# Kernel tuning notes

Hardware: AMD Instinct MI355X
Metric: run time of the kernel (lower is better)

## Reference

```python
import jax, jax.numpy as jnp
import numpy as np

EPS = 1e-10


def setup_inputs() -> dict:
    key = jax.random.key(0)
    k1, k2 = jax.random.split(key)
    supports = jax.random.normal(k1, (32, 512, 1024), dtype=jnp.float32)
    targets = jax.random.normal(k2, (32, 512, 1024), dtype=jnp.float32)
    return {"supports": supports, "targets": targets}


def reference(supports, targets):
    # targets: [B, T, D], supports: [B, S, D] -> sim: [B, T, S]
    # F.cosine_similarity(a, b, eps): dot / max(||a||*||b||, eps)
    dots = jnp.einsum("btd,bsd->bts", targets, supports)
    t_norm = jnp.linalg.norm(targets, axis=-1)   # [B, T]
    s_norm = jnp.linalg.norm(supports, axis=-1)  # [B, S]
    denom = jnp.maximum(t_norm[:, :, None] * s_norm[:, None, :], EPS)
    sim = dots / denom
    # normalize=True default: map (-1, 1) -> (0, 1)
    return (sim + 1.0) * 0.5
```

## Files before the change

### kernel.cpp

```cpp
#include <hip/hip_runtime.h>
#include <hip/hip_bf16.h>

typedef __attribute__((ext_vector_type(8))) short short8;
typedef __attribute__((ext_vector_type(4))) float f32x4;

#define NBATCH 32
#define NT 512
#define NS 512
#define ND 1024
#define BM 128
#define BN 256
#define BK 32
#define NK (ND / BK)

__device__ __forceinline__ short f2bf(float f) {
    union { __hip_bfloat16 h; short s; } u;
    u.h = __float2bfloat16(f);
    return u.s;
}

__device__ __forceinline__ short8 cvt8(float4 a, float4 b) {
    short8 r;
    r[0] = f2bf(a.x); r[1] = f2bf(a.y); r[2] = f2bf(a.z); r[3] = f2bf(a.w);
    r[4] = f2bf(b.x); r[5] = f2bf(b.y); r[6] = f2bf(b.z); r[7] = f2bf(b.w);
    return r;
}

__device__ __forceinline__ float ssq4(float s, float4 a) {
    return fmaf(a.x, a.x, fmaf(a.y, a.y, fmaf(a.z, a.z, fmaf(a.w, a.w, s))));
}

__global__ __launch_bounds__(512, 2)
void paircos_mfma(const float* __restrict__ sup, const float* __restrict__ tgt,
                  float* __restrict__ out) {
    __shared__ __align__(16) short As[2][BM * BK];
    __shared__ __align__(16) short Bs[2][BN * BK];
    __shared__ float tn[BM];
    __shared__ float sn[BN];

    const int tid = threadIdx.x;
    const int l    = blockIdx.x;
    const int wgid = (l & 7) * 32 + (l >> 3);
    const int b    = wgid >> 3;
    const int til  = wgid & 7;
    const int bt0  = (til >> 1) * BM;
    const int bs0  = (til & 1) * BN;

    const int seg  = tid & 3;
    const int srow = tid >> 2;

    const float* gA = tgt + (size_t)b * NT * ND + (size_t)(bt0 + srow) * ND + seg * 8;
    const float* gB = sup + (size_t)b * NS * ND + (size_t)(bs0 + srow) * ND + seg * 8;

    const int wave = tid >> 6;
    const int lane = tid & 63;
    const int wr  = (wave >> 2) * 64;
    const int wc  = (wave & 3) * 64;
    const int lhi = lane >> 4;
    const int llo = lane & 15;

    f32x4 acc[4][4];
#pragma unroll
    for (int m = 0; m < 4; ++m)
#pragma unroll
        for (int n = 0; n < 4; ++n)
            acc[m][n] = (f32x4){0.f, 0.f, 0.f, 0.f};

    float sqa = 0.f, sqb0 = 0.f, sqb1 = 0.f;

    float4 pA0, pA1, pB0, pB1, pB2, pB3;

    const int pu   = ((seg + (srow >> 1)) & 3) * 8;
    const int offw = srow * BK + pu;

#define LOADT(KK)                                                              \
    do {                                                                       \
        pA0 = *reinterpret_cast<const float4*>(gA + (KK) * BK);                \
        pA1 = *reinterpret_cast<const float4*>(gA + (KK) * BK + 4);            \
        pB0 = *reinterpret_cast<const float4*>(gB + (KK) * BK);                \
        pB1 = *reinterpret_cast<const float4*>(gB + (KK) * BK + 4);            \
        pB2 = *reinterpret_cast<const float4*>(gB + (KK) * BK + 128 * ND);     \
        pB3 = *reinterpret_cast<const float4*>(gB + (KK) * BK + 128 * ND + 4); \
    } while (0)

#define STORET(P)                                                              \
    do {                                                                       \
        sqa  = ssq4(ssq4(sqa,  pA0), pA1);                                     \
        *reinterpret_cast<short8*>(&As[P][offw]) = cvt8(pA0, pA1);             \
        sqb0 = ssq4(ssq4(sqb0, pB0), pB1);                                     \
        *reinterpret_cast<short8*>(&Bs[P][offw]) = cvt8(pB0, pB1);             \
        sqb1 = ssq4(ssq4(sqb1, pB2), pB3);                                     \
        *reinterpret_cast<short8*>(&Bs[P][offw + 128 * BK]) = cvt8(pB2, pB3);  \
    } while (0)

#define FRAG_READ(P)                                                           \
    do {                                                                       \
        _Pragma("unroll") for (int m = 0; m < 4; ++m) {                        \
            const int row = wr + m * 16 + llo;                                 \
            const int off = row * BK + (((lhi + (row >> 1)) & 3) * 8);         \
            af[m] = *reinterpret_cast<const short8*>(&As[P][off]);             \
        }                                                                      \
        _Pragma("unroll") for (int n = 0; n < 4; ++n) {                        \
            const int row = wc + n * 16 + llo;                                 \
            const int off = row * BK + (((lhi + (row >> 1)) & 3) * 8);         \
            bfr[n] = *reinterpret_cast<const short8*>(&Bs[P][off]);            \
        }                                                                      \
    } while (0)

#define MFMA_BLOCK()                                                           \
    do {                                                                       \
        __builtin_amdgcn_s_setprio(1);                                         \
        _Pragma("unroll") for (int m = 0; m < 4; ++m)                          \
            _Pragma("unroll") for (int n = 0; n < 4; ++n)                      \
                acc[m][n] = __builtin_amdgcn_mfma_f32_16x16x32_bf16(           \
                    af[m], bfr[n], acc[m][n], 0, 0, 0);                        \
        __builtin_amdgcn_s_setprio(0);                                         \
    } while (0)

#define PHASE_FENCE()                                                          \
    do {                                                                       \
        asm volatile("s_waitcnt lgkmcnt(0)" ::: "memory");                     \
        __builtin_amdgcn_s_barrier();                                          \
        asm volatile("" ::: "memory");                                         \
    } while (0)

    LOADT(0);
    STORET(0);
    LOADT(1);
    PHASE_FENCE();

    for (int k = 0; k < NK; ++k) {
        const int cur = k & 1;
        short8 af[4], bfr[4];
        FRAG_READ(cur);
        if (k + 1 < NK) STORET(cur ^ 1);
        if (k + 2 < NK) LOADT(k + 2);
        MFMA_BLOCK();
        PHASE_FENCE();
    }

    sqa  += __shfl_xor(sqa, 1);
    sqa  += __shfl_xor(sqa, 2);
    sqb0 += __shfl_xor(sqb0, 1);
    sqb0 += __shfl_xor(sqb0, 2);
    sqb1 += __shfl_xor(sqb1, 1);
    sqb1 += __shfl_xor(sqb1, 2);
    if (seg == 0) {
        tn[srow]       = sqrtf(sqa);
        sn[srow]       = sqrtf(sqb0);
        sn[srow + 128] = sqrtf(sqb1);
    }
    __syncthreads();

    float* outp = out + (size_t)b * NT * NS;
#pragma unroll
    for (int m = 0; m < 4; ++m) {
        const int lr0 = wr + m * 16 + lhi * 4;
#pragma unroll
        for (int n = 0; n < 4; ++n) {
            const int lc = wc + n * 16 + llo;
            const float snv = sn[lc];
            const int col = bs0 + lc;
#pragma unroll
            for (int j = 0; j < 4; ++j) {
                const float denom = fmaxf(tn[lr0 + j] * snv, 1e-10f);
                outp[(size_t)(bt0 + lr0 + j) * NS + col] =
                    acc[m][n][j] / denom * 0.5f + 0.5f;
            }
        }
    }
}

extern "C" void kernel_launch(void* const* d_in, const int* in_sizes, int n_in,
                              void* d_out, int out_size, void* d_ws, size_t ws_size,
                              hipStream_t stream) {
    const float* sup = (const float*)d_in[0];
    const float* tgt = (const float*)d_in[1];
    float* out = (float*)d_out;
    (void)in_sizes; (void)n_in; (void)out_size; (void)d_ws; (void)ws_size;
    paircos_mfma<<<dim3(32 * 8), 512, 0, stream>>>(sup, tgt, out);
}
```

Measured before the change: 35.15 us.

## Triple-buffer LDS and prefetch MFMA fragments one step ahead

Moves the K-loop from double to triple LDS buffering and reads the next tile's fragments into registers before issuing the current tile's MFMAs, unrolling by two with ping-pong register sets. The goal is to hide LDS read latency behind the MFMA chain, so the matrix core no longer waits on ds_read at the start of each step. This adds 50% more shared memory and an extra set of fragment registers, which could hurt occupancy at the requested two blocks per CU.

```diff
diff --git a/kernel.cpp b/kernel.cpp
--- a/kernel.cpp
+++ b/kernel.cpp
@@ -12,6 +12,8 @@
 #define BN 256
 #define BK 32
 #define NK (ND / BK)
+#define ATSZ (BM * BK)
+#define BTSZ (BN * BK)
 
 __device__ __forceinline__ short f2bf(float f) {
     union { __hip_bfloat16 h; short s; } u;
@@ -33,8 +35,8 @@
 __global__ __launch_bounds__(512, 2)
 void paircos_mfma(const float* __restrict__ sup, const float* __restrict__ tgt,
                   float* __restrict__ out) {
-    __shared__ __align__(16) short As[2][BM * BK];
-    __shared__ __align__(16) short Bs[2][BN * BK];
+    __shared__ __align__(16) short As[3 * ATSZ];
+    __shared__ __align__(16) short Bs[3 * BTSZ];
     __shared__ float tn[BM];
     __shared__ float sn[BN];
 
@@ -69,6 +71,7 @@
     float sqa = 0.f, sqb0 = 0.f, sqb1 = 0.f;
 
     float4 pA0, pA1, pB0, pB1, pB2, pB3;
+    short8 xa[4], xb[4], ya[4], yb[4];
 
     const int pu   = ((seg + (srow >> 1)) & 3) * 8;
     const int offw = srow * BK + pu;
@@ -83,37 +86,38 @@
         pB3 = *reinterpret_cast<const float4*>(gB + (KK) * BK + 128 * ND + 4); \
     } while (0)
 
-#define STORET(P)                                                              \
+#define STORET(WB)                                                             \
     do {                                                                       \
         sqa  = ssq4(ssq4(sqa,  pA0), pA1);                                     \
-        *reinterpret_cast<short8*>(&As[P][offw]) = cvt8(pA0, pA1);             \
+        *reinterpret_cast<short8*>(&As[(WB) * ATSZ + offw]) = cvt8(pA0, pA1);  \
         sqb0 = ssq4(ssq4(sqb0, pB0), pB1);                                     \
-        *reinterpret_cast<short8*>(&Bs[P][offw]) = cvt8(pB0, pB1);             \
+        *reinterpret_cast<short8*>(&Bs[(WB) * BTSZ + offw]) = cvt8(pB0, pB1);  \
         sqb1 = ssq4(ssq4(sqb1, pB2), pB3);                                     \
-        *reinterpret_cast<short8*>(&Bs[P][offw + 128 * BK]) = cvt8(pB2, pB3);  \
+        *reinterpret_cast<short8*>(&Bs[(WB) * BTSZ + offw + 128 * BK]) =       \
+            cvt8(pB2, pB3);                                                    \
     } while (0)
 
-#define FRAG_READ(P)                                                           \
+#define FRAG_READ(FA, FB, RB)                                                  \
     do {                                                                       \
         _Pragma("unroll") for (int m = 0; m < 4; ++m) {                        \
             const int row = wr + m * 16 + llo;                                 \
-            const int off = row * BK + (((lhi + (row >> 1)) & 3) * 8);         \
-            af[m] = *reinterpret_cast<const short8*>(&As[P][off]);             \
+            const int off = (RB) * ATSZ + row * BK + (((lhi + (row >> 1)) & 3) * 8); \
+            FA[m] = *reinterpret_cast<const short8*>(&As[off]);                \
         }                                                                      \
         _Pragma("unroll") for (int n = 0; n < 4; ++n) {                        \
             const int row = wc + n * 16 + llo;                                 \
-            const int off = row * BK + (((lhi + (row >> 1)) & 3) * 8);         \
-            bfr[n] = *reinterpret_cast<const short8*>(&Bs[P][off]);            \
+            const int off = (RB) * BTSZ + row * BK + (((lhi + (row >> 1)) & 3) * 8); \
+            FB[n] = *reinterpret_cast<const short8*>(&Bs[off]);                \
         }                                                                      \
     } while (0)
 
-#define MFMA_BLOCK()                                                           \
+#define MFMA_BLOCK(FA, FB)                                                     \
     do {                                                                       \
         __builtin_amdgcn_s_setprio(1);                                         \
         _Pragma("unroll") for (int m = 0; m < 4; ++m)                          \
             _Pragma("unroll") for (int n = 0; n < 4; ++n)                      \
                 acc[m][n] = __builtin_amdgcn_mfma_f32_16x16x32_bf16(           \
-                    af[m], bfr[n], acc[m][n], 0, 0, 0);                        \
+                    FA[m], FB[n], acc[m][n], 0, 0, 0);                         \
         __builtin_amdgcn_s_setprio(0);                                         \
     } while (0)
 
@@ -124,19 +128,32 @@
         asm volatile("" ::: "memory");                                         \
     } while (0)
 
+#define ROTATE()                                                               \
+    do { int t_ = cbuf; cbuf = rbuf; rbuf = wbuf; wbuf = t_; } while (0)
+
     LOADT(0);
     STORET(0);
     LOADT(1);
     PHASE_FENCE();
+    STORET(1);
+    LOADT(2);
+    FRAG_READ(xa, xb, 0);
+    PHASE_FENCE();
+    int cbuf = 0, rbuf = 1, wbuf = 2;
 
-    for (int k = 0; k < NK; ++k) {
-        const int cur = k & 1;
-        short8 af[4], bfr[4];
-        FRAG_READ(cur);
-        if (k + 1 < NK) STORET(cur ^ 1);
-        if (k + 2 < NK) LOADT(k + 2);
-        MFMA_BLOCK();
+    for (int k = 0; k < NK; k += 2) {
+        if (k + 1 < NK) FRAG_READ(ya, yb, rbuf);
+        if (k + 2 < NK) STORET(wbuf);
+        if (k + 3 < NK) LOADT(k + 3);
+        MFMA_BLOCK(xa, xb);
         PHASE_FENCE();
+        ROTATE();
+        if (k + 2 < NK) FRAG_READ(xa, xb, rbuf);
+        if (k + 3 < NK) STORET(wbuf);
+        if (k + 4 < NK) LOADT(k + 4);
+        MFMA_BLOCK(ya, yb);
+        PHASE_FENCE();
+        ROTATE();
     }
 
     sqa  += __shfl_xor(sqa, 1);
```

Measured after the change: 36.66 us. 4.3% more time.

## Double workgroup to 1024 threads with 16 waves each owning 64x32 subtiles

Applied to the files above, without the earlier changes.

The workgroup grows from 512 to 1024 threads, so each of 16 waves computes a 64x32 output subtile instead of 64x64. Global loads of B are spread across all threads, and only the first 512 threads load A, which cuts per-thread register and accumulator pressure. More waves per CU are meant to hide load latency better. The cost is more waves contending at every barrier, fewer MFMAs per fragment read, and divergent loads in the A path. The launch bounds of (1024, 4) may also force register limits that cause spills.

```diff
diff --git a/kernel.cpp b/kernel.cpp
--- a/kernel.cpp
+++ b/kernel.cpp
@@ -30,7 +30,7 @@
     return fmaf(a.x, a.x, fmaf(a.y, a.y, fmaf(a.z, a.z, fmaf(a.w, a.w, s))));
 }
 
-__global__ __launch_bounds__(512, 2)
+__global__ __launch_bounds__(1024, 4)
 void paircos_mfma(const float* __restrict__ sup, const float* __restrict__ tgt,
                   float* __restrict__ out) {
     __shared__ __align__(16) short As[2][BM * BK];
@@ -48,49 +48,49 @@
 
     const int seg  = tid & 3;
     const int srow = tid >> 2;
+    const bool stA = (tid < 512);
 
+    const float* gB = sup + (size_t)b * NS * ND + (size_t)(bs0 + srow) * ND + seg * 8;
     const float* gA = tgt + (size_t)b * NT * ND + (size_t)(bt0 + srow) * ND + seg * 8;
-    const float* gB = sup + (size_t)b * NS * ND + (size_t)(bs0 + srow) * ND + seg * 8;
 
     const int wave = tid >> 6;
     const int lane = tid & 63;
-    const int wr  = (wave >> 2) * 64;
-    const int wc  = (wave & 3) * 64;
+    const int wr  = (wave >> 3) * 64;
+    const int wc  = (wave & 7) * 32;
     const int lhi = lane >> 4;
     const int llo = lane & 15;
 
-    f32x4 acc[4][4];
+    f32x4 acc[4][2];
 #pragma unroll
     for (int m = 0; m < 4; ++m)
 #pragma unroll
-        for (int n = 0; n < 4; ++n)
+        for (int n = 0; n < 2; ++n)
             acc[m][n] = (f32x4){0.f, 0.f, 0.f, 0.f};
 
-    float sqa = 0.f, sqb0 = 0.f, sqb1 = 0.f;
+    float sqa = 0.f, sqb = 0.f;
 
-    float4 pA0, pA1, pB0, pB1, pB2, pB3;
+    float4 pA0, pA1, pB0, pB1;
 
-    const int pu   = ((seg + (srow >> 1)) & 3) * 8;
-    const int offw = srow * BK + pu;
+    const int offw = srow * BK + (((seg + (srow >> 1)) & 3) * 8);
 
 #define LOADT(KK)                                                              \
     do {                                                                       \
-        pA0 = *reinterpret_cast<const float4*>(gA + (KK) * BK);                \
-        pA1 = *reinterpret_cast<const float4*>(gA + (KK) * BK + 4);            \
         pB0 = *reinterpret_cast<const float4*>(gB + (KK) * BK);                \
         pB1 = *reinterpret_cast<const float4*>(gB + (KK) * BK + 4);            \
-        pB2 = *reinterpret_cast<const float4*>(gB + (KK) * BK + 128 * ND);     \
-        pB3 = *reinterpret_cast<const float4*>(gB + (KK) * BK + 128 * ND + 4); \
+        if (stA) {                                                             \
+            pA0 = *reinterpret_cast<const float4*>(gA + (KK) * BK);            \
+            pA1 = *reinterpret_cast<const float4*>(gA + (KK) * BK + 4);        \
+        }                                                                      \
     } while (0)
 
 #define STORET(P)                                                              \
     do {                                                                       \
-        sqa  = ssq4(ssq4(sqa,  pA0), pA1);                                     \
-        *reinterpret_cast<short8*>(&As[P][offw]) = cvt8(pA0, pA1);             \
-        sqb0 = ssq4(ssq4(sqb0, pB0), pB1);                                     \
+        sqb = ssq4(ssq4(sqb, pB0), pB1);                                       \
         *reinterpret_cast<short8*>(&Bs[P][offw]) = cvt8(pB0, pB1);             \
-        sqb1 = ssq4(ssq4(sqb1, pB2), pB3);                                     \
-        *reinterpret_cast<short8*>(&Bs[P][offw + 128 * BK]) = cvt8(pB2, pB3);  \
+        if (stA) {                                                             \
+            sqa = ssq4(ssq4(sqa, pA0), pA1);                                   \
+            *reinterpret_cast<short8*>(&As[P][offw]) = cvt8(pA0, pA1);         \
+        }                                                                      \
     } while (0)
 
 #define FRAG_READ(P)                                                           \
@@ -100,7 +100,7 @@
             const int off = row * BK + (((lhi + (row >> 1)) & 3) * 8);         \
             af[m] = *reinterpret_cast<const short8*>(&As[P][off]);             \
         }                                                                      \
-        _Pragma("unroll") for (int n = 0; n < 4; ++n) {                        \
+        _Pragma("unroll") for (int n = 0; n < 2; ++n) {                        \
             const int row = wc + n * 16 + llo;                                 \
             const int off = row * BK + (((lhi + (row >> 1)) & 3) * 8);         \
             bfr[n] = *reinterpret_cast<const short8*>(&Bs[P][off]);            \
@@ -111,7 +111,7 @@
     do {                                                                       \
         __builtin_amdgcn_s_setprio(1);                                         \
         _Pragma("unroll") for (int m = 0; m < 4; ++m)                          \
-            _Pragma("unroll") for (int n = 0; n < 4; ++n)                      \
+            _Pragma("unroll") for (int n = 0; n < 2; ++n)                      \
                 acc[m][n] = __builtin_amdgcn_mfma_f32_16x16x32_bf16(           \
                     af[m], bfr[n], acc[m][n], 0, 0, 0);                        \
         __builtin_amdgcn_s_setprio(0);                                         \
@@ -131,7 +131,7 @@
 
     for (int k = 0; k < NK; ++k) {
         const int cur = k & 1;
-        short8 af[4], bfr[4];
+        short8 af[4], bfr[2];
         FRAG_READ(cur);
         if (k + 1 < NK) STORET(cur ^ 1);
         if (k + 2 < NK) LOADT(k + 2);
@@ -139,16 +139,13 @@
         PHASE_FENCE();
     }
 
-    sqa  += __shfl_xor(sqa, 1);
-    sqa  += __shfl_xor(sqa, 2);
-    sqb0 += __shfl_xor(sqb0, 1);
-    sqb0 += __shfl_xor(sqb0, 2);
-    sqb1 += __shfl_xor(sqb1, 1);
-    sqb1 += __shfl_xor(sqb1, 2);
-    if (seg == 0) {
-        tn[srow]       = sqrtf(sqa);
-        sn[srow]       = sqrtf(sqb0);
-        sn[srow + 128] = sqrtf(sqb1);
+    sqb += __shfl_xor(sqb, 1);
+    sqb += __shfl_xor(sqb, 2);
+    if (seg == 0) sn[srow] = sqrtf(sqb);
+    if (stA) {
+        sqa += __shfl_xor(sqa, 1);
+        sqa += __shfl_xor(sqa, 2);
+        if (seg == 0) tn[srow] = sqrtf(sqa);
     }
     __syncthreads();
 
@@ -157,7 +154,7 @@
     for (int m = 0; m < 4; ++m) {
         const int lr0 = wr + m * 16 + lhi * 4;
 #pragma unroll
-        for (int n = 0; n < 4; ++n) {
+        for (int n = 0; n < 2; ++n) {
             const int lc = wc + n * 16 + llo;
             const float snv = sn[lc];
             const int col = bs0 + lc;
@@ -178,5 +175,5 @@
     const float* tgt = (const float*)d_in[1];
     float* out = (float*)d_out;
     (void)in_sizes; (void)n_in; (void)out_size; (void)d_ws; (void)ws_size;
-    paircos_mfma<<<dim3(32 * 8), 512, 0, stream>>>(sup, tgt, out);
+    paircos_mfma<<<dim3(32 * 8), 1024, 0, stream>>>(sup, tgt, out);
 }
```

New measurement: 34.37 us. 1.02x faster.
